# Kernel optimization log

Hardware: AMD Instinct MI355X
Metric: run time of the kernel (lower is better)

Reference implementation:

```python
import jax, jax.numpy as jnp
import numpy as np

B = 512    # batch of signals
N = 1024   # time samples per signal
M = 16384  # frequency grid points (super-resolved)


def setup_inputs() -> dict:
    key = jax.random.key(0)
    x = jax.random.normal(key, (B, 2, N), dtype=jnp.float32)  # [B, 2(re/im), N]
    xgrid = jnp.linspace(-0.5, 0.5, M, dtype=jnp.float32)      # normalized freqs
    return {"x": x, "xgrid": xgrid}


def reference(x, xgrid):
    # x: [B, 2, N] -> complex signal a + i*b
    # Periodogram at arbitrary freqs f: P(f) = |sum_n x_n * exp(-2j*pi*f*n)|^2 / N
    a = x[:, 0]  # real part [B, N]
    b = x[:, 1]  # imag part [B, N]
    Nn = x.shape[-1]
    n = jnp.arange(Nn, dtype=x.dtype)
    phase = (2.0 * jnp.pi) * xgrid[:, None] * n[None, :]  # [M, N]
    C = jnp.cos(phase)  # [M, N]
    S = jnp.sin(phase)  # [M, N]
    # x_n * (cos - i sin) = (a c + b s) + i (b c - a s)
    re = jnp.einsum('bn,mn->bm', a, C) + jnp.einsum('bn,mn->bm', b, S)
    im = jnp.einsum('bn,mn->bm', b, C) - jnp.einsum('bn,mn->bm', a, S)
    return (re * re + im * im) / Nn  # [B, M]
```

## Files before the change

### kernel.cpp

```cpp
#include <hip/hip_runtime.h>


typedef __fp16 half8  __attribute__((ext_vector_type(8)));
typedef __fp16 half2v __attribute__((ext_vector_type(2)));
typedef float  f32x4  __attribute__((ext_vector_type(4)));

#define B_SZ 512
#define N_SZ 1024
#define M_SZ 16384
#define BT 128
#define MT 128
#define KT 32
#define WS_ARR 1048576

union U4 { half2v h2[4]; uint4 u; };
union BF { half2v h2[4]; half8 v; uint4 u; };

__global__ __launch_bounds__(256)
void cvt_kernel(const float* __restrict__ x, unsigned char* __restrict__ ws) {
    const int id  = (int)blockIdx.x * 256 + (int)threadIdx.x;
    const int arr = id >> 16;
    const int rem = id & 65535;
    const int rb  = rem >> 11;
    const int kc  = (rem >> 6) & 31;
    const int l6  = rem & 63;
    const int r16 = l6 >> 2;
    const int g   = l6 & 3;
    const float* src = x + (size_t)(rb * 16 + r16) * 2048 + arr * 1024 + kc * 32 + g * 8;
    const float4 v0 = *(const float4*)src;
    const float4 v1 = *(const float4*)(src + 4);
    U4 u;
    u.h2[0] = __builtin_amdgcn_cvt_pkrtz(v0.x, v0.y);
    u.h2[1] = __builtin_amdgcn_cvt_pkrtz(v0.z, v0.w);
    u.h2[2] = __builtin_amdgcn_cvt_pkrtz(v1.x, v1.y);
    u.h2[3] = __builtin_amdgcn_cvt_pkrtz(v1.z, v1.w);
    *(uint4*)(ws + (size_t)arr * WS_ARR + (size_t)(rb * 32 + kc) * 1024 + (g * 16 + r16) * 16) = u.u;
}

__global__ __launch_bounds__(256, 2)
void periodogram_kernel(const unsigned char* __restrict__ ws,
                        const float* __restrict__ xgrid,
                        float* __restrict__ out) {
    const int tid  = (int)threadIdx.x;
    const int lane = tid & 63;
    const int w    = tid >> 6;
    const int bid  = (int)blockIdx.x;
    const int b0 = (bid & 3) * BT;
    const int m0 = (bid >> 2) * MT;

    const int wr = (w >> 1) * 64;
    const int wc = (w & 1) * 64;

    const unsigned char* pA[4];
    const unsigned char* pB[4];
#pragma unroll
    for (int fm = 0; fm < 4; ++fm) {
        const int rb = ((b0 + wr) >> 4) + fm;
        pA[fm] = ws + (size_t)(rb * 32) * 1024 + (size_t)(lane * 16);
        pB[fm] = pA[fm] + WS_ARR;
    }

    half2v PC[4][4], PS[4][4];
    float c0v[4], s0v[4], C32[4], S32[4];
    const float g8f = (float)((lane >> 4) << 3);
#pragma unroll
    for (int fn = 0; fn < 4; ++fn) {
        const float xg = xgrid[m0 + wc + fn * 16 + (lane & 15)];
        float Cj[8], Sj[8];
        Cj[0] = 1.0f; Sj[0] = 0.0f;
#pragma unroll
        for (int j = 1; j < 8; ++j) {
            float p = xg * (float)j; p -= floorf(p);
            Cj[j] = __builtin_amdgcn_cosf(p);
            Sj[j] = __builtin_amdgcn_sinf(p);
        }
#pragma unroll
        for (int i = 0; i < 4; ++i) {
            PC[fn][i] = __builtin_amdgcn_cvt_pkrtz(Cj[2 * i], Cj[2 * i + 1]);
            PS[fn][i] = __builtin_amdgcn_cvt_pkrtz(Sj[2 * i], Sj[2 * i + 1]);
        }
        float p32 = xg * 32.0f; p32 -= floorf(p32);
        C32[fn] = __builtin_amdgcn_cosf(p32);
        S32[fn] = __builtin_amdgcn_sinf(p32);
        float pb = xg * g8f; pb -= floorf(pb);
        c0v[fn] = __builtin_amdgcn_cosf(pb);
        s0v[fn] = __builtin_amdgcn_sinf(pb);
    }

    f32x4 accRe[4][4], accIm[4][4];
#pragma unroll
    for (int i = 0; i < 4; ++i)
#pragma unroll
        for (int j = 0; j < 4; ++j) { accRe[i][j] = (f32x4)0.0f; accIm[i][j] = (f32x4)0.0f; }

    for (int t = 0; t < N_SZ / KT; ++t) {
        half8 fa[4], fb[4];
        const unsigned off = (unsigned)(t * 1024);
#pragma unroll
        for (int fm = 0; fm < 4; ++fm) {
            fa[fm] = *(const half8*)(pA[fm] + off);
            fb[fm] = *(const half8*)(pB[fm] + off);
        }
#pragma unroll
        for (int fn = 0; fn < 4; ++fn) {
            const float c0 = c0v[fn], s0 = s0v[fn];
            const half2v c0b = __builtin_amdgcn_cvt_pkrtz(c0, c0);
            const half2v s0b = __builtin_amdgcn_cvt_pkrtz(s0, s0);
            BF fc, fs, fns;
#pragma unroll
            for (int i = 0; i < 4; ++i) {
                fc.h2[i] = c0b * PC[fn][i] - s0b * PS[fn][i];
                fs.h2[i] = s0b * PC[fn][i] + c0b * PS[fn][i];
            }
            fns.u.x = fs.u.x ^ 0x80008000u;
            fns.u.y = fs.u.y ^ 0x80008000u;
            fns.u.z = fs.u.z ^ 0x80008000u;
            fns.u.w = fs.u.w ^ 0x80008000u;
#pragma unroll
            for (int fm = 0; fm < 4; ++fm) {
                accRe[fm][fn] = __builtin_amdgcn_mfma_f32_16x16x32_f16(fa[fm], fc.v,  accRe[fm][fn], 0, 0, 0);
                accRe[fm][fn] = __builtin_amdgcn_mfma_f32_16x16x32_f16(fb[fm], fs.v,  accRe[fm][fn], 0, 0, 0);
                accIm[fm][fn] = __builtin_amdgcn_mfma_f32_16x16x32_f16(fb[fm], fc.v,  accIm[fm][fn], 0, 0, 0);
                accIm[fm][fn] = __builtin_amdgcn_mfma_f32_16x16x32_f16(fa[fm], fns.v, accIm[fm][fn], 0, 0, 0);
            }
            c0v[fn] = __builtin_fmaf(c0, C32[fn], -(s0 * S32[fn]));
            s0v[fn] = __builtin_fmaf(s0, C32[fn],  (c0 * S32[fn]));
        }
    }

    const float inv = 1.0f / (float)N_SZ;
    const int orow0 = b0 + wr + ((lane >> 4) << 2);
    const int ocol0 = m0 + wc + (lane & 15);
#pragma unroll
    for (int fm = 0; fm < 4; ++fm)
#pragma unroll
        for (int fn = 0; fn < 4; ++fn) {
            const f32x4 r = accRe[fm][fn];
            const f32x4 im = accIm[fm][fn];
            const int col = ocol0 + fn * 16;
#pragma unroll
            for (int j = 0; j < 4; ++j) {
                const int row = orow0 + fm * 16 + j;
                out[(size_t)row * M_SZ + col] = (r[j] * r[j] + im[j] * im[j]) * inv;
            }
        }
}

extern "C" void kernel_launch(void* const* d_in, const int* in_sizes, int n_in,
                              void* d_out, int out_size, void* d_ws, size_t ws_size,
                              hipStream_t stream) {
    const float* x     = (const float*)d_in[0];
    const float* xgrid = (const float*)d_in[1];
    float* out = (float*)d_out;
    unsigned char* ws = (unsigned char*)d_ws;
    cvt_kernel<<<512, 256, 0, stream>>>(x, ws);
    dim3 grid(B_SZ / BT * (M_SZ / MT));
    dim3 block(256);
    periodogram_kernel<<<grid, block, 0, stream>>>(ws, xgrid, out);
}
```

Baseline: 65.37 us.

## Double-buffer A/B fragments through LDS via async global_load_lds prefetch

Each wave now prefetches the next K-step's fp16 signal fragments straight into a private double-buffered LDS region using global_load_lds, then reads the current step's fragments from LDS. The goal is to overlap global-memory latency with the MFMA and twiddle work, where before each iteration loaded from global and had to wait on it. The cost is 64KB of shared memory per block, which can limit occupancy to one block per CU against the launch bound of two. The vmcnt(0) wait at the top of each iteration also still serializes on the prefetch.

```diff
diff --git a/kernel.cpp b/kernel.cpp
--- a/kernel.cpp
+++ b/kernel.cpp
@@ -11,10 +11,17 @@
 #define BT 128
 #define MT 128
 #define KT 32
+#define NT (N_SZ / KT)
 #define WS_ARR 1048576
 
 union U4 { half2v h2[4]; uint4 u; };
 union BF { half2v h2[4]; half8 v; uint4 u; };
+
+__device__ __forceinline__ void gld16(const void* g, void* l) {
+    __builtin_amdgcn_global_load_lds((__attribute__((address_space(1))) void*)g,
+                                     (__attribute__((address_space(3))) void*)l,
+                                     16, 0, 0);
+}
 
 __global__ __launch_bounds__(256)
 void cvt_kernel(const float* __restrict__ x, unsigned char* __restrict__ ws) {
@@ -41,6 +48,7 @@
 void periodogram_kernel(const unsigned char* __restrict__ ws,
                         const float* __restrict__ xgrid,
                         float* __restrict__ out) {
+    __shared__ __align__(16) unsigned char smem[65536];
     const int tid  = (int)threadIdx.x;
     const int lane = tid & 63;
     const int w    = tid >> 6;
@@ -50,6 +58,8 @@
 
     const int wr = (w >> 1) * 64;
     const int wc = (w & 1) * 64;
+
+    unsigned char* lb = smem + (unsigned)(w * 16384);
 
     const unsigned char* pA[4];
     const unsigned char* pB[4];
@@ -93,13 +103,29 @@
 #pragma unroll
         for (int j = 0; j < 4; ++j) { accRe[i][j] = (f32x4)0.0f; accIm[i][j] = (f32x4)0.0f; }
 
-    for (int t = 0; t < N_SZ / KT; ++t) {
+#pragma unroll
+    for (int fm = 0; fm < 4; ++fm) {
+        gld16(pA[fm], lb + (unsigned)(fm * 1024));
+        gld16(pB[fm], lb + (unsigned)(4096 + fm * 1024));
+    }
+
+    for (int t = 0; t < NT; ++t) {
+        const unsigned cb = (unsigned)(t & 1) * 8192u;
+        asm volatile("s_waitcnt vmcnt(0)" ::: "memory");
         half8 fa[4], fb[4];
-        const unsigned off = (unsigned)(t * 1024);
 #pragma unroll
         for (int fm = 0; fm < 4; ++fm) {
-            fa[fm] = *(const half8*)(pA[fm] + off);
-            fb[fm] = *(const half8*)(pB[fm] + off);
+            fa[fm] = *(const half8*)(lb + cb + (unsigned)(fm * 1024) + (unsigned)(lane * 16));
+            fb[fm] = *(const half8*)(lb + cb + (unsigned)(4096 + fm * 1024) + (unsigned)(lane * 16));
+        }
+        if (t < NT - 1) {
+            const unsigned nb = cb ^ 8192u;
+            const unsigned off = (unsigned)((t + 1) * 1024);
+#pragma unroll
+            for (int fm = 0; fm < 4; ++fm) {
+                gld16(pA[fm] + off, lb + nb + (unsigned)(fm * 1024));
+                gld16(pB[fm] + off, lb + nb + (unsigned)(4096 + fm * 1024));
+            }
         }
 #pragma unroll
         for (int fn = 0; fn < 4; ++fn) {
```

Measured after the change: 66.73 us. +2.1%, slower.
